# Performance work log

Measured on AMD Instinct MI355X. Metric: run time of the kernel, lower is better.

The kernel has to match this reference:

```python
import jax, jax.numpy as jnp
import numpy as np
import math

B, S, D, O_DIM = 8, 2048, 1024, 1024

def setup_inputs() -> dict:
    key = jax.random.key(0)
    ks = jax.random.split(key, 4)
    scale = 1.0 / math.sqrt(D)
    return {
        "x": jax.random.normal(ks[0], (B, S, D), dtype=jnp.float32),
        "Wq": jax.random.normal(ks[1], (D, O_DIM), dtype=jnp.float32) * scale,
        "bq": jnp.zeros((O_DIM,), dtype=jnp.float32),
        "Wk": jax.random.normal(ks[2], (D, O_DIM), dtype=jnp.float32) * scale,
        "bk": jnp.zeros((O_DIM,), dtype=jnp.float32),
        "Wv": jax.random.normal(ks[3], (D, O_DIM), dtype=jnp.float32) * scale,
        "bv": jnp.zeros((O_DIM,), dtype=jnp.float32),
    }

def reference(x, Wq, bq, Wk, bk, Wv, bv):
    o_dim = Wq.shape[1]
    q = x @ Wq + bq  # [B,S,O]
    k = x @ Wk + bk
    v = x @ Wv + bv
    scores = jnp.einsum('bid,bjd->bij', q, k) / jnp.sqrt(jnp.float32(o_dim))
    n = scores.shape[1]
    # causal additive mask: upper triangle (j > i) gets -1e20 added
    causal = jnp.tril(jnp.ones((n, n), dtype=scores.dtype))
    scores = scores + (1.0 - causal) * (-1e20)
    probs = jax.nn.softmax(scores, axis=-1)
    return jnp.einsum('bij,bjd->bid', probs, v)
```

## Files before the change

kernel.cpp:

```cpp
#include <hip/hip_runtime.h>

typedef unsigned short u16;
typedef unsigned int u32;
typedef __attribute__((ext_vector_type(8))) short short8;
typedef __attribute__((ext_vector_type(4))) float floatx4;

__device__ __forceinline__ u16 f2bf(float f) {
  u32 u = __float_as_uint(f);
  return (u16)((u + 0x7FFFu + ((u >> 16) & 1u)) >> 16);
}

__device__ __forceinline__ float bf2f(u16 b) {
  return __uint_as_float(((u32)b) << 16);
}

__device__ __forceinline__ void gload16(const void* g, void* l) {
  __builtin_amdgcn_global_load_lds((const __attribute__((address_space(1))) void*)g,
                                   (__attribute__((address_space(3))) void*)l, 16, 0, 0);
}

template<int BIAS_MODE, bool OUT_BF16, bool CAUSAL, bool KLIMIT, int SWZ>
__global__ __launch_bounds__(512, 2)
void gemm256(const u16* __restrict__ A, int lda, long strideA,
             const u16* __restrict__ B, int ldb, long strideB,
             void* __restrict__ Cv, int ldc, long strideC,
             const float* __restrict__ bias, float scale, int K)
{
  int bx = blockIdx.x, by = blockIdx.y;
  if (SWZ == 1) {
    const int c = gridDim.x >> 3;
    bx = (bx & 7) * c + (bx >> 3);
  } else if (SWZ == 2) {
    const u32 gx = gridDim.x;
    const u32 flat = (u32)by * gx + (u32)bx;
    const u32 j = flat & 7u, w = flat >> 3;
    const u32 rpx = gridDim.y >> 3;
    by = (int)(j * rpx + w / gx);
    bx = (int)(w % gx);
  }
  const int rb = by * 256, cb = bx * 256;
  if (CAUSAL && cb > rb + 255) return;

  A += (long)blockIdx.z * strideA;
  B += (long)blockIdx.z * strideB;
  const long coff = (long)blockIdx.z * strideC;

  __shared__ __align__(16) char lds[131072];

  const int t = threadIdx.x;
  const int lane = t & 63, wid = t >> 6;
  const int wr = wid >> 2, wc = wid & 3;

  floatx4 acc[8][4];
#pragma unroll
  for (int i = 0; i < 8; ++i)
#pragma unroll
    for (int j = 0; j < 4; ++j) acc[i][j] = (floatx4)(0.0f);

  const int sr = t >> 2;
  const int sl = (t & 3) ^ ((sr >> 1) & 3);
  const u16* Ag0 = A + (long)(rb + sr) * lda + sl * 8;
  const u16* Ag1 = A + (long)(rb + sr + 128) * lda + sl * 8;
  const u16* Bg0 = B + (long)(cb + sr) * ldb + sl * 8;
  const u16* Bg1 = B + (long)(cb + sr + 128) * ldb + sl * 8;

#define STAGE_A(T) { const long ko_ = (long)(T) * 32;                          \
    char* d_ = lds + (((T) & 3) << 15) + (wid << 10);                          \
    gload16(Ag0 + ko_, d_); gload16(Ag1 + ko_, d_ + 8192); }
#define STAGE_B(T) { const long ko_ = (long)(T) * 32;                          \
    char* d_ = lds + (((T) & 3) << 15) + 16384 + (wid << 10);                  \
    gload16(Bg0 + ko_, d_); gload16(Bg1 + ko_, d_ + 8192); }

  const int g = lane >> 4;
  int aoff[8], boff[4];
  const int arow = wr * 128 + (lane & 15);
  const int brow = wc * 64 + (lane & 15);
#pragma unroll
  for (int i = 0; i < 8; ++i) {
    const int ra = arow + i * 16;
    aoff[i] = ra * 64 + ((g ^ ((ra >> 1) & 3)) * 16);
  }
#pragma unroll
  for (int j = 0; j < 4; ++j) {
    const int rbq = brow + j * 16;
    boff[j] = rbq * 64 + ((g ^ ((rbq >> 1) & 3)) * 16);
  }

  int kend = K;
  if (KLIMIT) kend = (rb + 256 < K) ? (rb + 256) : K;
  const int NT = kend / 32;

  STAGE_A(0); STAGE_B(0);
  STAGE_A(1); STAGE_B(1);
  STAGE_A(2); STAGE_B(2);
  asm volatile("s_waitcnt vmcnt(8)" ::: "memory");
  __builtin_amdgcn_s_barrier();
  asm volatile("" ::: "memory");

  for (int T = 0; T < NT; ++T) {
    const char* bufA = lds + ((T & 3) << 15);
    const char* bufB = bufA + 16384;

    if (T + 3 < NT) STAGE_A(T + 3);
    short8 a0[4], bfr[4];
#pragma unroll
    for (int i = 0; i < 4; ++i) a0[i] = *(const short8*)(bufA + aoff[i]);
#pragma unroll
    for (int j = 0; j < 4; ++j) bfr[j] = *(const short8*)(bufB + boff[j]);
    __builtin_amdgcn_s_setprio(1);
#pragma unroll
    for (int mi = 0; mi < 4; ++mi)
#pragma unroll
      for (int nj = 0; nj < 4; ++nj)
        acc[mi][nj] = __builtin_amdgcn_mfma_f32_16x16x32_bf16(a0[mi], bfr[nj], acc[mi][nj], 0, 0, 0);
    __builtin_amdgcn_s_setprio(0);

    if (T + 3 < NT) STAGE_B(T + 3);
    short8 a1[4];
#pragma unroll
    for (int i = 0; i < 4; ++i) a1[i] = *(const short8*)(bufA + aoff[4 + i]);
    __builtin_amdgcn_s_setprio(1);
#pragma unroll
    for (int mi = 0; mi < 4; ++mi)
#pragma unroll
      for (int nj = 0; nj < 4; ++nj)
        acc[4 + mi][nj] = __builtin_amdgcn_mfma_f32_16x16x32_bf16(a1[mi], bfr[nj], acc[4 + mi][nj], 0, 0, 0);
    __builtin_amdgcn_s_setprio(0);

    asm volatile("" ::: "memory");
    if (T < NT - 3) {
      asm volatile("s_waitcnt vmcnt(8)" ::: "memory");
      __builtin_amdgcn_s_barrier();
    } else if (T == NT - 3) {
      asm volatile("s_waitcnt vmcnt(4)" ::: "memory");
      __builtin_amdgcn_s_barrier();
    } else if (T == NT - 2) {
      asm volatile("s_waitcnt vmcnt(0)" ::: "memory");
      __builtin_amdgcn_s_barrier();
    }
    asm volatile("" ::: "memory");
  }
#undef STAGE_A
#undef STAGE_B

#pragma unroll
  for (int mi = 0; mi < 8; ++mi) {
    const int r0 = rb + wr * 128 + mi * 16 + (lane >> 4) * 4;
#pragma unroll
    for (int nj = 0; nj < 4; ++nj) {
      const int c = cb + wc * 64 + nj * 16 + (lane & 15);
      float bc = 0.0f;
      if (BIAS_MODE == 1) bc = bias[c];
#pragma unroll
      for (int e = 0; e < 4; ++e) {
        const int r = r0 + e;
        float val = acc[mi][nj][e] * scale + bc;
        if (BIAS_MODE == 2) val += bias[r];
        const long idx = coff + (long)r * ldc + c;
        if (OUT_BF16) ((u16*)Cv)[idx] = f2bf(val);
        else          ((float*)Cv)[idx] = val;
      }
    }
  }
}

__global__ __launch_bounds__(256)
void softmax_causal_bf16(u16* __restrict__ Pp, int n, long stride)
{
  const int i = blockIdx.x;
  u16* row = Pp + (long)blockIdx.y * stride + (long)i * n;
  const int t = threadIdx.x;
  const int lane = t & 63, wid = t >> 6;
  const int jb = t * 8;

  float v[8];
  const bool any = (jb <= i);
  if (any) {
    short8 sv = *(const short8*)(row + jb);
#pragma unroll
    for (int e = 0; e < 8; ++e) v[e] = bf2f((u16)sv[e]);
  } else {
#pragma unroll
    for (int e = 0; e < 8; ++e) v[e] = 0.0f;
  }

  float mx = -3.0e38f;
#pragma unroll
  for (int e = 0; e < 8; ++e) if (any && jb + e <= i) mx = fmaxf(mx, v[e]);
#pragma unroll
  for (int off = 32; off > 0; off >>= 1) mx = fmaxf(mx, __shfl_xor(mx, off));
  __shared__ float red[8];
  if (lane == 0) red[wid] = mx;
  __syncthreads();
  mx = fmaxf(fmaxf(red[0], red[1]), fmaxf(red[2], red[3]));

  float s = 0.0f;
#pragma unroll
  for (int e = 0; e < 8; ++e) {
    float p = (any && jb + e <= i) ? __expf(v[e] - mx) : 0.0f;
    v[e] = p; s += p;
  }
#pragma unroll
  for (int off = 32; off > 0; off >>= 1) s += __shfl_xor(s, off);
  if (lane == 0) red[4 + wid] = s;
  __syncthreads();
  s = red[4] + red[5] + red[6] + red[7];
  const float inv = 1.0f / s;

  short8 o;
#pragma unroll
  for (int e = 0; e < 8; ++e) o[e] = (short)f2bf(v[e] * inv);
  *(short8*)(row + jb) = o;
}

__global__ __launch_bounds__(256)
void transpose_conv3(const float* __restrict__ Wq, const float* __restrict__ Wk,
                     const float* __restrict__ Wv, u16* __restrict__ WqkT,
                     u16* __restrict__ WvT, int dim)
{
  const float* W;
  u16* WT;
  if (blockIdx.z == 0)      { W = Wq; WT = WqkT; }
  else if (blockIdx.z == 1) { W = Wk; WT = WqkT + (long)dim * dim; }
  else                      { W = Wv; WT = WvT; }

  __shared__ float tile[32][33];
  const int tx = threadIdx.x & 31;
  const int ty = threadIdx.x >> 5;
  const int c0 = blockIdx.x * 32;
  const int r0 = blockIdx.y * 32;
#pragma unroll
  for (int i = 0; i < 4; ++i)
    tile[ty + 8 * i][tx] = W[(long)(r0 + ty + 8 * i) * dim + c0 + tx];
  __syncthreads();
#pragma unroll
  for (int i = 0; i < 4; ++i)
    WT[(long)(c0 + ty + 8 * i) * dim + r0 + tx] = f2bf(tile[tx][ty + 8 * i]);
}

__global__ __launch_bounds__(256)
void conv_bf16(const float* __restrict__ X, u16* __restrict__ Xb, long n8)
{
  const long i = (long)blockIdx.x * 256 + threadIdx.x;
  if (i >= n8) return;
  const float4* s = (const float4*)X + i * 2;
  float4 a = s[0], b = s[1];
  short8 o;
  o[0] = (short)f2bf(a.x); o[1] = (short)f2bf(a.y);
  o[2] = (short)f2bf(a.z); o[3] = (short)f2bf(a.w);
  o[4] = (short)f2bf(b.x); o[5] = (short)f2bf(b.y);
  o[6] = (short)f2bf(b.z); o[7] = (short)f2bf(b.w);
  ((short8*)Xb)[i] = o;
}

__global__ __launch_bounds__(256)
void pack_bias2(const float* __restrict__ b0, const float* __restrict__ b1,
                float* __restrict__ dst, int n)
{
  const int i = blockIdx.x * 256 + threadIdx.x;
  if (i < n) dst[i] = b0[i];
  else if (i < 2 * n) dst[i] = b1[i - n];
}

extern "C" void kernel_launch(void* const* d_in, const int* in_sizes, int n_in,
                              void* d_out, int out_size, void* d_ws, size_t ws_size,
                              hipStream_t stream)
{
  const int Bb = 8, S = 2048, Dd = 1024, Od = 1024;
  const int M = Bb * S;

  const float* x  = (const float*)d_in[0];
  const float* Wq = (const float*)d_in[1];
  const float* bq = (const float*)d_in[2];
  const float* Wk = (const float*)d_in[3];
  const float* bk = (const float*)d_in[4];
  const float* Wv = (const float*)d_in[5];
  const float* bv = (const float*)d_in[6];
  float* out = (float*)d_out;

  char* ws = (char*)d_ws;
  u16* xb   = (u16*)(ws);
  u16* qk   = (u16*)(ws + 33554432L);
  u16* vT   = (u16*)(ws + 100663296L);
  u16* WqkT = (u16*)(ws + 134217728L);
  u16* WvT  = (u16*)(ws + 138412032L);
  float* bqk = (float*)(ws + 140509184L);
  const size_t attn_base = 140517376UL;

  conv_bf16<<<dim3(8192), dim3(256), 0, stream>>>(x, xb, (long)M * Dd / 8);
  transpose_conv3<<<dim3(32, 32, 3), dim3(256), 0, stream>>>(Wq, Wk, Wv, WqkT, WvT, Dd);
  pack_bias2<<<dim3(8), dim3(256), 0, stream>>>(bq, bk, bqk, Od);

  gemm256<1, true, false, false, 2><<<dim3(2 * Od / 256, M / 256), dim3(512), 0, stream>>>(
      xb, Dd, 0L, WqkT, Dd, 0L, qk, 2 * Od, 0L, bqk, 1.0f, Dd);
  gemm256<2, true, false, false, 1><<<dim3(M / 256, Od / 256), dim3(512), 0, stream>>>(
      WvT, Dd, 0L, xb, Dd, 0L, vT, M, 0L, bv, 1.0f, Dd);

  const u16* qb = qk;
  const u16* kb = qk + Od;
  const int ldqk = 2 * Od;
  const long strideQK = (long)S * ldqk;
  const long sS = (long)S * S;

  u16* scores;
  int g;
  if (ws_size >= attn_base + 8UL * (size_t)sS * sizeof(u16)) {
    scores = (u16*)(ws + attn_base);
    g = 8;
  } else {
    scores = xb;
    g = 4;
  }

  const float sc = 0.03125f;
  for (int b0 = 0; b0 < Bb; b0 += g) {
    const int gz = (b0 + g <= Bb) ? g : (Bb - b0);
    gemm256<0, true, true, false, 0><<<dim3(S / 256, S / 256, gz), dim3(512), 0, stream>>>(
        qb + (long)b0 * strideQK, ldqk, strideQK,
        kb + (long)b0 * strideQK, ldqk, strideQK,
        scores, S, sS, nullptr, sc, Od);
    softmax_causal_bf16<<<dim3(S, gz), dim3(256), 0, stream>>>(scores, S, sS);
    gemm256<0, false, false, true, 0><<<dim3(Od / 256, S / 256, gz), dim3(512), 0, stream>>>(
        scores, S, sS, vT + (long)b0 * S, M, (long)S,
        out + (long)b0 * S * Od, Od, (long)S * Od, nullptr, 1.0f, S);
  }
}
```

Before: 407.2 us.

## Add dedicated small-LDS causal scores kernel, fuse prep kernels, trim softmax writes

Replaces the causal QK^T GEMM instance with a dedicated scores256 kernel that uses a 32 KB single-stage LDS buffer instead of the 128 KB general tile, so more blocks can be resident per CU while skipping upper-triangle tiles. The three preprocessing kernels (x conversion, weight transpose, bias packing) are merged into one launch to cut launch overhead. Softmax now only writes probabilities up to the end of the row's 256-column tile, skipping stores the PV GEMM never reads. In exchange, the new scores kernel has no software pipelining and synchronises twice per K step, which may expose global-load latency.

```diff
diff --git a/kernel.cpp b/kernel.cpp
--- a/kernel.cpp
+++ b/kernel.cpp
@@ -19,7 +19,7 @@
                                    (__attribute__((address_space(3))) void*)l, 16, 0, 0);
 }
 
-template<int BIAS_MODE, bool OUT_BF16, bool CAUSAL, bool KLIMIT, int SWZ>
+template<int BIAS_MODE, bool OUT_BF16, bool KLIMIT, int SWZ>
 __global__ __launch_bounds__(512, 2)
 void gemm256(const u16* __restrict__ A, int lda, long strideA,
              const u16* __restrict__ B, int ldb, long strideB,
@@ -39,7 +39,6 @@
     bx = (int)(w % gx);
   }
   const int rb = by * 256, cb = bx * 256;
-  if (CAUSAL && cb > rb + 255) return;
 
   A += (long)blockIdx.z * strideA;
   B += (long)blockIdx.z * strideB;
@@ -164,6 +163,96 @@
   }
 }
 
+__global__ __launch_bounds__(512)
+void scores256(const u16* __restrict__ A, int lda, long strideA,
+               const u16* __restrict__ B, int ldb, long strideB,
+               u16* __restrict__ C, int ldc, long strideC,
+               float scale, int K)
+{
+  const int rb = blockIdx.y * 256, cb = blockIdx.x * 256;
+  if (cb > rb + 255) return;
+
+  A += (long)blockIdx.z * strideA;
+  B += (long)blockIdx.z * strideB;
+  const long coff = (long)blockIdx.z * strideC;
+
+  __shared__ __align__(16) char lds[32768];
+
+  const int t = threadIdx.x;
+  const int lane = t & 63, wid = t >> 6;
+  const int wr = wid >> 2, wc = wid & 3;
+
+  floatx4 acc[8][4];
+#pragma unroll
+  for (int i = 0; i < 8; ++i)
+#pragma unroll
+    for (int j = 0; j < 4; ++j) acc[i][j] = (floatx4)(0.0f);
+
+  const int sr = t >> 2;
+  const int sl = (t & 3) ^ ((sr >> 1) & 3);
+  const u16* Ag0 = A + (long)(rb + sr) * lda + sl * 8;
+  const u16* Ag1 = A + (long)(rb + sr + 128) * lda + sl * 8;
+  const u16* Bg0 = B + (long)(cb + sr) * ldb + sl * 8;
+  const u16* Bg1 = B + (long)(cb + sr + 128) * ldb + sl * 8;
+
+  const int g = lane >> 4;
+  int aoff[8], boff[4];
+  const int arow = wr * 128 + (lane & 15);
+  const int brow = wc * 64 + (lane & 15);
+#pragma unroll
+  for (int i = 0; i < 8; ++i) {
+    const int ra = arow + i * 16;
+    aoff[i] = ra * 64 + ((g ^ ((ra >> 1) & 3)) * 16);
+  }
+#pragma unroll
+  for (int j = 0; j < 4; ++j) {
+    const int rbq = brow + j * 16;
+    boff[j] = rbq * 64 + ((g ^ ((rbq >> 1) & 3)) * 16);
+  }
+
+  const int NT = K / 32;
+  for (int T = 0; T < NT; ++T) {
+    const long ko = (long)T * 32;
+    char* dA = lds + (wid << 10);
+    char* dB = lds + 16384 + (wid << 10);
+    gload16(Ag0 + ko, dA); gload16(Ag1 + ko, dA + 8192);
+    gload16(Bg0 + ko, dB); gload16(Bg1 + ko, dB + 8192);
+    __syncthreads();
+    short8 a0[4], a1[4], bfr[4];
+#pragma unroll
+    for (int i = 0; i < 4; ++i) {
+      a0[i] = *(const short8*)((const char*)lds + aoff[i]);
+      a1[i] = *(const short8*)((const char*)lds + aoff[4 + i]);
+      bfr[i] = *(const short8*)((const char*)lds + 16384 + boff[i]);
+    }
+#pragma unroll
+    for (int mi = 0; mi < 4; ++mi)
+#pragma unroll
+      for (int nj = 0; nj < 4; ++nj)
+        acc[mi][nj] = __builtin_amdgcn_mfma_f32_16x16x32_bf16(a0[mi], bfr[nj], acc[mi][nj], 0, 0, 0);
+#pragma unroll
+    for (int mi = 0; mi < 4; ++mi)
+#pragma unroll
+      for (int nj = 0; nj < 4; ++nj)
+        acc[4 + mi][nj] = __builtin_amdgcn_mfma_f32_16x16x32_bf16(a1[mi], bfr[nj], acc[4 + mi][nj], 0, 0, 0);
+    __syncthreads();
+  }
+
+#pragma unroll
+  for (int mi = 0; mi < 8; ++mi) {
+    const int r0 = rb + wr * 128 + mi * 16 + (lane >> 4) * 4;
+#pragma unroll
+    for (int nj = 0; nj < 4; ++nj) {
+      const int c = cb + wc * 64 + nj * 16 + (lane & 15);
+#pragma unroll
+      for (int e = 0; e < 4; ++e) {
+        const int r = r0 + e;
+        C[coff + (long)r * ldc + c] = f2bf(acc[mi][nj][e] * scale);
+      }
+    }
+  }
+}
+
 __global__ __launch_bounds__(256)
 void softmax_causal_bf16(u16* __restrict__ Pp, int n, long stride)
 {
@@ -172,6 +261,7 @@
   const int t = threadIdx.x;
   const int lane = t & 63, wid = t >> 6;
   const int jb = t * 8;
+  const int tile_end = ((i >> 8) + 1) << 8;
 
   float v[8];
   const bool any = (jb <= i);
@@ -207,59 +297,58 @@
   s = red[4] + red[5] + red[6] + red[7];
   const float inv = 1.0f / s;
 
-  short8 o;
-#pragma unroll
-  for (int e = 0; e < 8; ++e) o[e] = (short)f2bf(v[e] * inv);
-  *(short8*)(row + jb) = o;
+  if (jb < tile_end) {
+    short8 o;
+#pragma unroll
+    for (int e = 0; e < 8; ++e) o[e] = (short)f2bf(v[e] * inv);
+    *(short8*)(row + jb) = o;
+  }
 }
 
 __global__ __launch_bounds__(256)
-void transpose_conv3(const float* __restrict__ Wq, const float* __restrict__ Wk,
-                     const float* __restrict__ Wv, u16* __restrict__ WqkT,
-                     u16* __restrict__ WvT, int dim)
+void prep(const float* __restrict__ x, const float* __restrict__ Wq,
+          const float* __restrict__ Wk, const float* __restrict__ Wv,
+          const float* __restrict__ bq, const float* __restrict__ bk,
+          u16* __restrict__ xb, u16* __restrict__ WqkT, u16* __restrict__ WvT,
+          float* __restrict__ bqk, int dim, long n8)
 {
-  const float* W;
-  u16* WT;
-  if (blockIdx.z == 0)      { W = Wq; WT = WqkT; }
-  else if (blockIdx.z == 1) { W = Wk; WT = WqkT + (long)dim * dim; }
-  else                      { W = Wv; WT = WvT; }
-
+  const int b = blockIdx.x;
   __shared__ float tile[32][33];
-  const int tx = threadIdx.x & 31;
-  const int ty = threadIdx.x >> 5;
-  const int c0 = blockIdx.x * 32;
-  const int r0 = blockIdx.y * 32;
-#pragma unroll
-  for (int i = 0; i < 4; ++i)
-    tile[ty + 8 * i][tx] = W[(long)(r0 + ty + 8 * i) * dim + c0 + tx];
-  __syncthreads();
-#pragma unroll
-  for (int i = 0; i < 4; ++i)
-    WT[(long)(c0 + ty + 8 * i) * dim + r0 + tx] = f2bf(tile[tx][ty + 8 * i]);
-}
-
-__global__ __launch_bounds__(256)
-void conv_bf16(const float* __restrict__ X, u16* __restrict__ Xb, long n8)
-{
-  const long i = (long)blockIdx.x * 256 + threadIdx.x;
-  if (i >= n8) return;
-  const float4* s = (const float4*)X + i * 2;
-  float4 a = s[0], b = s[1];
-  short8 o;
-  o[0] = (short)f2bf(a.x); o[1] = (short)f2bf(a.y);
-  o[2] = (short)f2bf(a.z); o[3] = (short)f2bf(a.w);
-  o[4] = (short)f2bf(b.x); o[5] = (short)f2bf(b.y);
-  o[6] = (short)f2bf(b.z); o[7] = (short)f2bf(b.w);
-  ((short8*)Xb)[i] = o;
-}
-
-__global__ __launch_bounds__(256)
-void pack_bias2(const float* __restrict__ b0, const float* __restrict__ b1,
-                float* __restrict__ dst, int n)
-{
-  const int i = blockIdx.x * 256 + threadIdx.x;
-  if (i < n) dst[i] = b0[i];
-  else if (i < 2 * n) dst[i] = b1[i - n];
+  if (b < 8192) {
+    const long i = (long)b * 256 + threadIdx.x;
+    if (i >= n8) return;
+    const float4* s = (const float4*)x + i * 2;
+    float4 a = s[0], c = s[1];
+    short8 o;
+    o[0] = (short)f2bf(a.x); o[1] = (short)f2bf(a.y);
+    o[2] = (short)f2bf(a.z); o[3] = (short)f2bf(a.w);
+    o[4] = (short)f2bf(c.x); o[5] = (short)f2bf(c.y);
+    o[6] = (short)f2bf(c.z); o[7] = (short)f2bf(c.w);
+    ((short8*)xb)[i] = o;
+  } else if (b < 11264) {
+    const int idx = b - 8192;
+    const int z = idx >> 10, rem = idx & 1023;
+    const float* W;
+    u16* WT;
+    if (z == 0)      { W = Wq; WT = WqkT; }
+    else if (z == 1) { W = Wk; WT = WqkT + (long)dim * dim; }
+    else             { W = Wv; WT = WvT; }
+    const int tx = threadIdx.x & 31;
+    const int ty = threadIdx.x >> 5;
+    const int c0 = (rem & 31) * 32;
+    const int r0 = (rem >> 5) * 32;
+#pragma unroll
+    for (int i = 0; i < 4; ++i)
+      tile[ty + 8 * i][tx] = W[(long)(r0 + ty + 8 * i) * dim + c0 + tx];
+    __syncthreads();
+#pragma unroll
+    for (int i = 0; i < 4; ++i)
+      WT[(long)(c0 + ty + 8 * i) * dim + r0 + tx] = f2bf(tile[tx][ty + 8 * i]);
+  } else {
+    const int i = (b - 11264) * 256 + threadIdx.x;
+    if (i < dim) bqk[i] = bq[i];
+    else if (i < 2 * dim) bqk[i] = bk[i - dim];
+  }
 }
 
 extern "C" void kernel_launch(void* const* d_in, const int* in_sizes, int n_in,
@@ -287,13 +376,13 @@
   float* bqk = (float*)(ws + 140509184L);
   const size_t attn_base = 140517376UL;
 
-  conv_bf16<<<dim3(8192), dim3(256), 0, stream>>>(x, xb, (long)M * Dd / 8);
-  transpose_conv3<<<dim3(32, 32, 3), dim3(256), 0, stream>>>(Wq, Wk, Wv, WqkT, WvT, Dd);
-  pack_bias2<<<dim3(8), dim3(256), 0, stream>>>(bq, bk, bqk, Od);
-
-  gemm256<1, true, false, false, 2><<<dim3(2 * Od / 256, M / 256), dim3(512), 0, stream>>>(
+  prep<<<dim3(11272), dim3(256), 0, stream>>>(x, Wq, Wk, Wv, bq, bk,
+                                              xb, WqkT, WvT, bqk, Dd,
+                                              (long)M * Dd / 8);
+
+  gemm256<1, true, false, 2><<<dim3(2 * Od / 256, M / 256), dim3(512), 0, stream>>>(
       xb, Dd, 0L, WqkT, Dd, 0L, qk, 2 * Od, 0L, bqk, 1.0f, Dd);
-  gemm256<2, true, false, false, 1><<<dim3(M / 256, Od / 256), dim3(512), 0, stream>>>(
+  gemm256<2, true, false, 1><<<dim3(M / 256, Od / 256), dim3(512), 0, stream>>>(
       WvT, Dd, 0L, xb, Dd, 0L, vT, M, 0L, bv, 1.0f, Dd);
 
   const u16* qb = qk;
@@ -315,12 +404,12 @@
   const float sc = 0.03125f;
   for (int b0 = 0; b0 < Bb; b0 += g) {
     const int gz = (b0 + g <= Bb) ? g : (Bb - b0);
-    gemm256<0, true, true, false, 0><<<dim3(S / 256, S / 256, gz), dim3(512), 0, stream>>>(
+    scores256<<<dim3(S / 256, S / 256, gz), dim3(512), 0, stream>>>(
         qb + (long)b0 * strideQK, ldqk, strideQK,
         kb + (long)b0 * strideQK, ldqk, strideQK,
-        scores, S, sS, nullptr, sc, Od);
+        scores, S, sS, sc, Od);
     softmax_causal_bf16<<<dim3(S, gz), dim3(256), 0, stream>>>(scores, S, sS);
-    gemm256<0, false, false, true, 0><<<dim3(Od / 256, S / 256, gz), dim3(512), 0, stream>>>(
+    gemm256<0, false, true, 0><<<dim3(Od / 256, S / 256, gz), dim3(512), 0, stream>>>(
         scores, S, sS, vT + (long)b0 * S, M, (long)S,
         out + (long)b0 * S * Od, Od, (long)S * Od, nullptr, 1.0f, S);
   }
```

Result: no change. 413.8 us (+1.6%).
